# Kernel optimization log

Measured on AMD Instinct MI355X. Metric: run time of the kernel, lower is better.

Reference implementation:

```python
import jax, jax.numpy as jnp
import numpy as np

S, I, CM, C, D, CZ = 128, 512, 256, 32, 32, 128
EPS = 1e-5


def setup_inputs() -> dict:
    key = jax.random.key(0)
    ks = jax.random.split(key, 7)
    x = jax.random.normal(ks[0], (1, S, I, CM), dtype=jnp.float32)
    norm_w = 1.0 + 0.1 * jax.random.normal(ks[1], (CM,), dtype=jnp.float32)
    norm_b = 0.1 * jax.random.normal(ks[2], (CM,), dtype=jnp.float32)
    Wa = jax.random.normal(ks[3], (C, CM), dtype=jnp.float32) / np.sqrt(CM)
    Wb = jax.random.normal(ks[4], (D, CM), dtype=jnp.float32) / np.sqrt(CM)
    Wo = jax.random.normal(ks[5], (CZ, C * D), dtype=jnp.float32) / np.sqrt(C * D)
    bo = 0.1 * jax.random.normal(ks[6], (CZ,), dtype=jnp.float32)
    return {"x": x, "norm_w": norm_w, "norm_b": norm_b, "Wa": Wa, "Wb": Wb, "Wo": Wo, "bo": bo}


def reference(x, norm_w, norm_b, Wa, Wb, Wo, bo):
    m = x[0]                                   # [S, I, CM] (drop leading batch dim)
    mu = jnp.mean(m, axis=-1, keepdims=True)
    var = jnp.mean((m - mu) ** 2, axis=-1, keepdims=True)
    ln = (m - mu) * jax.lax.rsqrt(var + EPS) * norm_w + norm_b
    a = jnp.einsum('sim,cm->sic', ln, Wa)      # [S, I, C]
    b = jnp.einsum('sjm,dm->sjd', ln, Wb)      # [S, J, D]
    s = a.shape[0]
    # outer product mean over S: [I, J, C, D]; flatten order is (c, d) -> c*D + d,
    # matching the reshape(chunk, C, J, D) -> permute(0,2,1,3) -> flatten in the original.
    o = jnp.einsum('sic,sjd->ijcd', a, b) * (1.0 / s)
    z = o.reshape(o.shape[0], o.shape[1], C * D) @ Wo.T + bo  # [I, J, CZ]
    return z[None]                             # [1, I, J, CZ]
```

## Files before the change

### kernel.cpp

```cpp
#include <hip/hip_runtime.h>

#define EPS 1e-5f

typedef _Float16 half8 __attribute__((ext_vector_type(8)));
typedef _Float16 half4 __attribute__((ext_vector_type(4)));
typedef float f32x4 __attribute__((ext_vector_type(4)));
typedef float f32x16 __attribute__((ext_vector_type(16)));

#define AB_STRIDE 72
#define AB_CHUNK  (16384 * AB_STRIDE)

__device__ __forceinline__ void load16_to_lds(const void* g, void* l) {
    __builtin_amdgcn_global_load_lds((__attribute__((address_space(1))) void*)g,
                                     (__attribute__((address_space(3))) void*)l, 16, 0, 0);
}

__global__ __launch_bounds__(256)
void k_cvt(const float* __restrict__ Wo, const float* __restrict__ Wa,
           const float* __restrict__ Wb, _Float16* __restrict__ WoH,
           _Float16* __restrict__ WabH)
{
    __shared__ _Float16 tile[32 * 36];
    const int t = threadIdx.x;
    if (blockIdx.x < 128) {
        const int n = blockIdx.x;
        float4 v = *(const float4*)(Wo + (size_t)n * 1024 + t * 4);
        int c  = t >> 3;
        int d0 = (t * 4) & 31;
        tile[(d0 + 0) * 36 + c] = (_Float16)v.x;
        tile[(d0 + 1) * 36 + c] = (_Float16)v.y;
        tile[(d0 + 2) * 36 + c] = (_Float16)v.z;
        tile[(d0 + 3) * 36 + c] = (_Float16)v.w;
        __syncthreads();
        int d  = t >> 3;
        int c0 = (t * 4) & 31;
        half4 o = *(const half4*)(tile + d * 36 + c0);
        *(half4*)(WoH + (size_t)n * 1024 + t * 4) = o;
    } else {
        int idx = ((blockIdx.x - 128) * 256 + t) * 4;
        const float* src = (idx < 8192) ? (Wa + idx) : (Wb + (idx - 8192));
        float4 v = *(const float4*)src;
        half4 h;
        h[0] = (_Float16)v.x; h[1] = (_Float16)v.y; h[2] = (_Float16)v.z; h[3] = (_Float16)v.w;
        *(half4*)(WabH + idx) = h;
    }
}

__global__ __launch_bounds__(512, 4)
void k1_ln_proj(const float* __restrict__ x, const float* __restrict__ nw,
                const float* __restrict__ nb, const _Float16* __restrict__ WabH,
                _Float16* __restrict__ aT, _Float16* __restrict__ bT)
{
    __shared__ float    xraw[3 * 8 * 256];
    __shared__ _Float16 xln[64 * 264];
    __shared__ _Float16 oT[256 * 40];

    const int tid  = threadIdx.x;
    const int lane = tid & 63;
    const int w    = tid >> 6;
    const int quad = lane >> 4;
    const int l15  = lane & 15;
    const int i0   = (blockIdx.x >> 2) * 4;
    const int sc   = blockIdx.x & 3;

    const int mt  = w & 3;
    const int ntg = w >> 2;

    const float4 gw = ((const float4*)nw)[lane];
    const float4 gb = ((const float4*)nb)[lane];

    auto src_of = [&](int c) -> const float* {
        int rl = ((c & 7) << 3) + w;
        int s_ = sc * 32 + ((c >> 3) << 4) + (rl >> 2);
        int i_ = i0 + (rl & 3);
        return x + ((size_t)s_ * 512 + i_) * 256;
    };

    load16_to_lds(src_of(0) + lane * 4, xraw + (0 * 8 + w) * 256 + lane * 4);
    load16_to_lds(src_of(1) + lane * 4, xraw + (1 * 8 + w) * 256 + lane * 4);

    int rb = 0;
    for (int half = 0; half < 2; ++half) {
        for (int cc = 0; cc < 8; ++cc) {
            const int c = half * 8 + cc;
            if (c == 15) asm volatile("s_waitcnt vmcnt(0)" ::: "memory");
            else         asm volatile("s_waitcnt vmcnt(1)" ::: "memory");

            const float4 v = *(const float4*)(xraw + (rb * 8 + w) * 256 + lane * 4);
            float sum = v.x + v.y + v.z + v.w;
            float ss  = v.x * v.x + v.y * v.y + v.z * v.z + v.w * v.w;
            #pragma unroll
            for (int off = 32; off > 0; off >>= 1) {
                sum += __shfl_xor(sum, off);
                ss  += __shfl_xor(ss, off);
            }
            float mu  = sum * (1.f / 256.f);
            float var = ss * (1.f / 256.f) - mu * mu;
            float rs  = rsqrtf(var + EPS);
            half4 o;
            o[0] = (_Float16)((v.x - mu) * rs * gw.x + gb.x);
            o[1] = (_Float16)((v.y - mu) * rs * gw.y + gb.y);
            o[2] = (_Float16)((v.z - mu) * rs * gw.z + gb.z);
            o[3] = (_Float16)((v.w - mu) * rs * gw.w + gb.w);
            int rl = (cc << 3) + w;
            *(half4*)(xln + rl * 264 + lane * 4) = o;

            if (c + 2 < 16) {
                int nb3 = rb + 2; if (nb3 >= 3) nb3 -= 3;
                load16_to_lds(src_of(c + 2) + lane * 4, xraw + (nb3 * 8 + w) * 256 + lane * 4);
            }
            ++rb; if (rb == 3) rb = 0;
        }
        asm volatile("s_waitcnt lgkmcnt(0)" ::: "memory");
        __builtin_amdgcn_s_barrier();

        f32x4 acc2[2] = {};
        #pragma unroll
        for (int kk = 0; kk < 8; ++kk) {
            half8 af = *(const half8*)(xln + (mt * 16 + l15) * 264 + kk * 32 + quad * 8);
            #pragma unroll
            for (int t = 0; t < 2; ++t) {
                half8 bf = *(const half8*)(WabH + (ntg * 32 + t * 16 + l15) * 256 + kk * 32 + quad * 8);
                acc2[t] = __builtin_amdgcn_mfma_f32_16x16x32_f16(af, bf, acc2[t], 0, 0, 0);
            }
        }

        #pragma unroll
        for (int t = 0; t < 2; ++t) {
            int c64  = ntg * 32 + t * 16 + l15;
            int base = ((c64 >= 32) ? 128 : 0) + (c64 & 31);
            int s_l  = half * 16 + mt * 4 + quad;
            #pragma unroll
            for (int r = 0; r < 4; ++r)
                oT[(base + r * 32) * 40 + s_l] = (_Float16)acc2[t][r];
        }
        asm volatile("s_waitcnt lgkmcnt(0)" ::: "memory");
        __builtin_amdgcn_s_barrier();
    }

    #pragma unroll
    for (int it2 = 0; it2 < 2; ++it2) {
        int u   = it2 * 512 + tid;
        int row = u >> 2;
        int off = (u & 3) * 8;
        half8 v = *(const half8*)(oT + row * 40 + off);
        _Float16* dst = (row < 128) ? aT : bT;
        int grow = i0 * 32 + (row & 127);
        *(half8*)(dst + (size_t)(sc >> 1) * AB_CHUNK + (size_t)grow * 72 + (sc & 1) * 32 + off) = v;
    }
}

__global__ __launch_bounds__(512, 4)
void k2_main(const _Float16* __restrict__ aT, const _Float16* __restrict__ bT,
             const _Float16* __restrict__ WoH, const float* __restrict__ bo,
             float* __restrict__ out)
{
    __shared__ _Float16 smem[33024];
    _Float16* sA = smem;
    _Float16* sB = smem + 256 * AB_STRIDE;
    _Float16* oL = smem;

    const int tid  = threadIdx.x;
    const int lane = tid & 63;
    const int w    = tid >> 6;
    const int quad = lane >> 4;
    const int l15  = lane & 15;
    const int wy   = w >> 1, wx = w & 1;

    const int wid = blockIdx.x;
    const int xcd = wid & 7;
    const int loc = wid >> 3;
    const int it  = (xcd >> 2) * 32 + (loc >> 5);
    const int jt  = (xcd & 3) * 32 + (loc & 31);

    const char* gA = (const char*)(aT + (size_t)it * 256 * AB_STRIDE);
    const char* gB = (const char*)(bT + (size_t)jt * 128 * AB_STRIDE);

    f32x4 acc[4][4] = {};

    for (int ck = 0; ck < 2; ++ck) {
        const char* cA = gA + (size_t)ck * (AB_CHUNK * 2);
        const char* cB = gB + (size_t)ck * (AB_CHUNK * 2);
        for (int seg = w; seg < 54; seg += 8) {
            if (seg < 36) load16_to_lds(cA + seg * 1024 + lane * 16, (char*)sA + seg * 1024 + lane * 16);
            else          load16_to_lds(cB + (seg - 36) * 1024 + lane * 16, (char*)sB + (seg - 36) * 1024 + lane * 16);
        }
        __syncthreads();

        #pragma unroll
        for (int kloc = 0; kloc < 2; ++kloc) {
            half8 af[4], bf[4];
            #pragma unroll
            for (int mt = 0; mt < 4; ++mt)
                af[mt] = *(const half8*)(sA + (wy * 64 + mt * 16 + l15) * AB_STRIDE + kloc * 32 + quad * 8);
            #pragma unroll
            for (int nt = 0; nt < 4; ++nt)
                bf[nt] = *(const half8*)(sB + (wx * 64 + nt * 16 + l15) * AB_STRIDE + kloc * 32 + quad * 8);
            #pragma unroll
            for (int mt = 0; mt < 4; ++mt)
                #pragma unroll
                for (int nt = 0; nt < 4; ++nt)
                    acc[mt][nt] = __builtin_amdgcn_mfma_f32_16x16x32_f16(af[mt], bf[nt], acc[mt][nt], 0, 0, 0);
        }
        __syncthreads();
    }

    #pragma unroll
    for (int mt = 0; mt < 4; ++mt) {
        int c0     = (mt & 1) * 16 + quad * 4;
        int chunk3 = (c0 >> 3);
        int il     = wy * 2 + (mt >> 1);
        #pragma unroll
        for (int nt = 0; nt < 4; ++nt) {
            int d    = (nt & 1) * 16 + l15;
            int jl   = wx * 2 + (nt >> 1);
            int pair = il * 4 + jl;
            int cS   = (c0 & 7) + ((chunk3 ^ ((d >> 1) & 3)) << 3);
            half4 v;
            v[0] = (_Float16)(acc[mt][nt][0] * (1.f / 128.f));
            v[1] = (_Float16)(acc[mt][nt][1] * (1.f / 128.f));
            v[2] = (_Float16)(acc[mt][nt][2] * (1.f / 128.f));
            v[3] = (_Float16)(acc[mt][nt][3] * (1.f / 128.f));
            *(half4*)(oL + pair * 1032 + d * 32 + cS) = v;
        }
    }
    __syncthreads();

    f32x16 zacc = {};
    const int nq = w & 3, kh = w >> 2;
    const int hi = lane >> 5;
    const int p32 = lane & 31;
    const _Float16* woB = WoH + (size_t)(nq * 32 + p32) * 1024;
    const _Float16* oaB = oL + p32 * 1032;
    const int qb = kh * 64 + hi;
    #pragma unroll 4
    for (int s = 0; s < 32; ++s) {
        int q   = qb + s * 2;
        int ach = (q & 3) ^ ((q >> 3) & 3);
        half8 oa = *(const half8*)(oaB + (q >> 2) * 32 + ach * 8);
        half8 wb = *(const half8*)(woB + q * 8);
        zacc = __builtin_amdgcn_mfma_f32_32x32x16_f16(oa, wb, zacc, 0, 0, 0);
    }
    __syncthreads();

    float* red = (float*)smem;
    if (kh == 1) {
        float* dst = red + (nq * 64 + lane) * 20;
        #pragma unroll
        for (int r4 = 0; r4 < 4; ++r4)
            *(f32x4*)(dst + r4 * 4) = ((f32x4*)&zacc)[r4];
    }
    __syncthreads();
    if (kh == 0) {
        const float* srcr = red + (nq * 64 + lane) * 20;
        float bias = bo[nq * 32 + p32];
        #pragma unroll
        for (int r = 0; r < 16; ++r) {
            int pair = (r & 3) + 8 * (r >> 2) + 4 * hi;
            int il = pair >> 2, jl = pair & 3;
            out[(((size_t)(it * 8 + il)) * 512 + jt * 4 + jl) * 128 + nq * 32 + p32]
                = zacc[r] + srcr[r] + bias;
        }
    }
}

extern "C" void kernel_launch(void* const* d_in, const int* in_sizes, int n_in,
                              void* d_out, int out_size, void* d_ws, size_t ws_size,
                              hipStream_t stream)
{
    const float* x      = (const float*)d_in[0];
    const float* norm_w = (const float*)d_in[1];
    const float* norm_b = (const float*)d_in[2];
    const float* Wa     = (const float*)d_in[3];
    const float* Wb     = (const float*)d_in[4];
    const float* Wo     = (const float*)d_in[5];
    const float* bo     = (const float*)d_in[6];
    float* out = (float*)d_out;

    _Float16* aT   = (_Float16*)d_ws;
    _Float16* bT   = aT + 2 * (size_t)AB_CHUNK;
    _Float16* WoH  = bT + 2 * (size_t)AB_CHUNK;
    _Float16* WabH = WoH + 131072;

    k_cvt<<<144, 256, 0, stream>>>(Wo, Wa, Wb, WoH, WabH);
    k1_ln_proj<<<512, 512, 0, stream>>>(x, norm_w, norm_b, WabH, aT, bT);
    k2_main<<<8192, 512, 0, stream>>>(aT, bT, WoH, bo, out);
}
```

Baseline: 476.4 us.

## Stage Wo weights through triple-buffered LDS ring with async global-to-LDS loads

Replaces direct per-lane global reads of the fp16 Wo matrix in the output projection with a three-slot LDS ring. Four waves prefetch slices using global_load_lds, and all waves consume them in lockstep with explicit waitcnt and barriers. The goal is to hide global load latency behind the MFMA work and to prefetch the first slices during the outer-product phase. The cost is 64 rounds of block-wide barriers, during which only half the waves issue an MFMA per step, plus extra LDS use that may reduce occupancy.

```diff
diff --git a/kernel.cpp b/kernel.cpp
--- a/kernel.cpp
+++ b/kernel.cpp
@@ -155,10 +155,11 @@
              const _Float16* __restrict__ WoH, const float* __restrict__ bo,
              float* __restrict__ out)
 {
-    __shared__ _Float16 smem[33024];
+    __shared__ _Float16 smem[39168];
     _Float16* sA = smem;
     _Float16* sB = smem + 256 * AB_STRIDE;
     _Float16* oL = smem;
+    _Float16* ring = smem + 33024;
 
     const int tid  = threadIdx.x;
     const int lane = tid & 63;
@@ -167,11 +168,27 @@
     const int l15  = lane & 15;
     const int wy   = w >> 1, wx = w & 1;
 
+    const int nq = w & 3, kh = w >> 2;
+    const int hi = lane >> 5;
+    const int p32 = lane & 31;
+
     const int wid = blockIdx.x;
     const int xcd = wid & 7;
     const int loc = wid >> 3;
     const int it  = (xcd >> 2) * 32 + (loc >> 5);
     const int jt  = (xcd & 3) * 32 + (loc & 31);
+
+    const float bias = bo[nq * 32 + p32];
+
+    if (w < 4) {
+        const int u = w >> 1;
+        const int row = (w & 1) * 64 + lane;
+        #pragma unroll
+        for (int pp = 0; pp < 3; ++pp) {
+            const _Float16* src = WoH + (size_t)row * 1024 + (pp & 1) * 512 + (pp >> 1) * 16 + u * 8;
+            load16_to_lds(src, ring + pp * 2048 + u * 1024 + row * 8);
+        }
+    }
 
     const char* gA = (const char*)(aT + (size_t)it * 256 * AB_STRIDE);
     const char* gB = (const char*)(bT + (size_t)jt * 128 * AB_STRIDE);
@@ -227,20 +244,49 @@
     __syncthreads();
 
     f32x16 zacc = {};
-    const int nq = w & 3, kh = w >> 2;
-    const int hi = lane >> 5;
-    const int p32 = lane & 31;
-    const _Float16* woB = WoH + (size_t)(nq * 32 + p32) * 1024;
     const _Float16* oaB = oL + p32 * 1032;
-    const int qb = kh * 64 + hi;
-    #pragma unroll 4
-    for (int s = 0; s < 32; ++s) {
-        int q   = qb + s * 2;
-        int ach = (q & 3) ^ ((q >> 3) & 3);
-        half8 oa = *(const half8*)(oaB + (q >> 2) * 32 + ach * 8);
-        half8 wb = *(const half8*)(woB + q * 8);
-        zacc = __builtin_amdgcn_mfma_f32_32x32x16_f16(oa, wb, zacc, 0, 0, 0);
-    }
+    const int brow = (nq * 32 + p32) * 8;
+    const int stg_u = w >> 1;
+    const int stg_row = (w & 1) * 64 + lane;
+
+    auto ring_compute = [&](int p) {
+        if ((p & 1) == kh) {
+            int s2  = p >> 1;
+            int q   = kh * 64 + s2 * 2 + hi;
+            int ach = (q & 3) ^ ((q >> 3) & 3);
+            half8 oa = *(const half8*)(oaB + (q >> 2) * 32 + ach * 8);
+            half8 wb = *(const half8*)(ring + (p % 3) * 2048 + hi * 1024 + brow);
+            zacc = __builtin_amdgcn_mfma_f32_32x32x16_f16(oa, wb, zacc, 0, 0, 0);
+        }
+    };
+
+    #pragma unroll 6
+    for (int p = 0; p < 62; ++p) {
+        asm volatile("s_waitcnt vmcnt(2)" ::: "memory");
+        __builtin_amdgcn_s_barrier();
+        asm volatile("" ::: "memory");
+        ring_compute(p);
+        asm volatile("s_waitcnt lgkmcnt(0)" ::: "memory");
+        __builtin_amdgcn_s_barrier();
+        asm volatile("" ::: "memory");
+        if (p < 61 && w < 4) {
+            int pn = p + 3;
+            const _Float16* src = WoH + (size_t)stg_row * 1024 + (pn & 1) * 512 + (pn >> 1) * 16 + stg_u * 8;
+            load16_to_lds(src, ring + (pn % 3) * 2048 + stg_u * 1024 + stg_row * 8);
+        }
+    }
+    asm volatile("s_waitcnt vmcnt(1)" ::: "memory");
+    __builtin_amdgcn_s_barrier();
+    asm volatile("" ::: "memory");
+    ring_compute(62);
+    asm volatile("s_waitcnt lgkmcnt(0)" ::: "memory");
+    __builtin_amdgcn_s_barrier();
+    asm volatile("" ::: "memory");
+    asm volatile("s_waitcnt vmcnt(0)" ::: "memory");
+    __builtin_amdgcn_s_barrier();
+    asm volatile("" ::: "memory");
+    ring_compute(63);
+
     __syncthreads();
 
     float* red = (float*)smem;
@@ -253,7 +299,6 @@
     __syncthreads();
     if (kh == 0) {
         const float* srcr = red + (nq * 64 + lane) * 20;
-        float bias = bo[nq * 32 + p32];
         #pragma unroll
         for (int r = 0; r < 16; ++r) {
             int pair = (r & 3) + 8 * (r >> 2) + 4 * hi;
```

After: 506.7 us. 1.06x slower.
